# Kernel optimization log

Measured on AMD Instinct MI355X. Metric: run time of the kernel, lower is better.

The kernel has to match this reference:

```python
import jax, jax.numpy as jnp
import numpy as np

WIND_SIZE = 5
EPSILON = 1e-5
ALPHA = 1.0


def _windows(a, w):
    # a: [B,1,H,W] -> [B, w*w, H, W], zero-padded, window index in (di,dj) row-major
    # order matching torch's unfold(dim=2).unfold(dim=3) + reshape.
    p = w // 2
    B, _, H, W = a.shape
    ap = jnp.pad(a[:, 0], ((0, 0), (p, p), (p, p)))
    taps = [ap[:, i:i + H, j:j + W] for i in range(w) for j in range(w)]
    return jnp.stack(taps, axis=1)


def setup_inputs() -> dict:
    key = jax.random.key(0)
    ks = jax.random.split(key, 6)
    B, H, W = 4, 512, 512
    ww = WIND_SIZE * WIND_SIZE
    fake = jax.random.uniform(ks[0], (B, 1, H, W), dtype=jnp.float32)
    gamma_hdr = jax.random.uniform(ks[1], (B, 1, H, W), dtype=jnp.float32)
    # strictly positive so hdr**(1-f) is well defined
    hdr_original_im = jax.random.uniform(ks[2], (B, 1, H, W), dtype=jnp.float32) + 0.01
    r_weights = jax.random.uniform(ks[3], (B, ww, H, W), dtype=jnp.float32)
    # f_factors in [0.5, 1.5] to avoid division blow-up, realistic gamma factors
    f_factors = jax.random.uniform(ks[4], (B,), dtype=jnp.float32) + 0.5
    hdr_original_gray = jax.random.uniform(ks[5], (B, 1, H, W), dtype=jnp.float32)
    return {
        'fake': fake,
        'gamma_hdr': gamma_hdr,
        'hdr_original_im': hdr_original_im,
        'r_weights': r_weights,
        'f_factors': f_factors,
        'hdr_original_gray': hdr_original_gray,
    }


def reference(fake, gamma_hdr, hdr_original_im, r_weights, f_factors, hdr_original_gray):
    w = WIND_SIZE
    eps = jnp.float32(EPSILON)
    # create_window -> uniform window, normalized: every tap weight = 1/(w*w)
    dist_gauss = jnp.float32(1.0 / (w * w))
    weights_map = dist_gauss * r_weights                      # [B, w*w, H, W]
    weights_map_sum = jnp.sum(weights_map, axis=1, keepdims=True)  # [B,1,H,W]

    def bf_stats(x):
        xw = _windows(x, w)                                   # [B, w*w, H, W]
        mu = jnp.sum(xw * weights_map, axis=1, keepdims=True) / weights_map_sum
        var = jnp.sum((xw - mu) ** 2 * weights_map, axis=1, keepdims=True) / weights_map_sum
        std = jnp.sqrt(jnp.maximum(var, 0.0) + eps)
        return mu, std

    _, std_fake = bf_stats(fake)
    _, std_gamma = bf_stats(gamma_hdr)

    ff = f_factors[:, None, None, None]                       # [B,1,1,1]
    hdr_pow = jnp.power(hdr_original_im, 1.0 - ff)
    hw = _windows(hdr_pow, w)
    hdr_pow_mu = jnp.sum(hw * weights_map, axis=1, keepdims=True) / weights_map_sum

    w_blf = jnp.sum(r_weights, axis=1, keepdims=True) - 1.0   # [B,1,H,W]

    std_objective = (ALPHA / ff) * std_gamma * (hdr_pow_mu + eps)
    gray_max = jnp.max(hdr_original_gray.reshape(hdr_original_gray.shape[0], -1), axis=1)
    std_objective = std_objective * gray_max[:, None, None, None]

    res = 1.0 - std_fake / (std_fake + jax.lax.stop_gradient(std_objective))
    res = res * (w_blf / jnp.mean(w_blf))
    return jnp.mean(res)
```

## Files before the change

### kernel.cpp

```cpp
#include <hip/hip_runtime.h>

#define Bn 4
#define Hn 512
#define Wn 512
#define HWn (Hn * Wn)

constexpr float kEps = 1e-5f;


__global__ __launch_bounds__(256) void gmax_kernel(
    const float* __restrict__ gray, float* __restrict__ gpart) {
  const int b = blockIdx.y;
  const int i = (blockIdx.x * 256 + threadIdx.x) << 2;
  const float4 g4 = *(const float4*)(gray + b * HWn + i);
  float lmax = fmaxf(fmaxf(g4.x, g4.y), fmaxf(g4.z, g4.w));
#pragma unroll
  for (int off = 32; off > 0; off >>= 1)
    lmax = fmaxf(lmax, __shfl_down(lmax, off));
  __shared__ float smax[4];
  const int lane = threadIdx.x & 63, wid = threadIdx.x >> 6;
  if (lane == 0) smax[wid] = lmax;
  __syncthreads();
  if (threadIdx.x == 0) {
    gpart[b * 256 + blockIdx.x] =
        fmaxf(fmaxf(smax[0], smax[1]), fmaxf(smax[2], smax[3]));
  }
}

__global__ __launch_bounds__(512, 4) void main_kernel(
    const float* __restrict__ fake, const float* __restrict__ gamma,
    const float* __restrict__ hdr, const float* __restrict__ rw,
    const float* __restrict__ ff, const float* __restrict__ gpart,
    float* __restrict__ s1part, float* __restrict__ s2part) {
  __shared__ float smem[3][8][512];
  __shared__ float sh1[8], sh2[8], sh_gm[4];

  const int b = blockIdx.x >> 7;
  const int h0 = (blockIdx.x & 127) << 2;
  const float e = 1.0f - ff[b];

  const float* fb = fake + (size_t)b * HWn;
  const float* gb = gamma + (size_t)b * HWn;
  const float* hb = hdr + (size_t)b * HWn;

  const int t = threadIdx.x;
  const int lr = t >> 7;
  const int w0 = (t & 127) << 2;
  const int h = h0 + lr;
  const float* rwb = rw + (size_t)b * 25 * HWn + (h << 9) + w0;

  float4 wv[5];
#pragma unroll
  for (int d = 0; d < 5; ++d)
    wv[d] = *(const float4*)(rwb + (size_t)d * HWn);

  if (t < 256) {
    float gm = gpart[(b << 8) + t];
#pragma unroll
    for (int off = 32; off > 0; off >>= 1)
      gm = fmaxf(gm, __shfl_down(gm, off));
    if ((t & 63) == 0) sh_gm[t >> 6] = gm;
  }

  float4* smem4 = (float4*)smem;
#pragma unroll
  for (int k = 0; k < 6; ++k) {
    const int i = t + (k << 9);
    const int a = i >> 10;
    const int rem = i & 1023;
    const int r = rem >> 7;
    const int c4 = rem & 127;
    const int grow = min(max(h0 - 2 + r, 0), Hn - 1);
    const float* src = (a == 0) ? fb : (a == 1) ? gb : hb;
    float4 v = *(const float4*)(src + (grow << 9) + (c4 << 2));
    if (a == 2) {
      v.x = __powf(v.x, e);
      v.y = __powf(v.y, e);
      v.z = __powf(v.z, e);
      v.w = __powf(v.w, e);
    }
    smem4[i] = v;
  }
  __syncthreads();

  float Sw[4] = {0, 0, 0, 0}, Sf[4] = {0, 0, 0, 0}, Sf2[4] = {0, 0, 0, 0};
  float Sg[4] = {0, 0, 0, 0}, Sg2[4] = {0, 0, 0, 0}, Sh[4] = {0, 0, 0, 0};

  float cm[12];
#pragma unroll
  for (int i = 2; i < 10; ++i)
    cm[i] = ((unsigned)(w0 - 4 + i) < (unsigned)Wn) ? 1.0f : 0.0f;
  const int c0 = max(w0 - 4, 0);
  const int c2 = min(w0 + 4, Wn - 4);

#pragma unroll
  for (int dyi = 0; dyi < 5; ++dyi) {
    const int r = lr + dyi;
    const float rmask = ((unsigned)(h + dyi - 2) < (unsigned)Hn) ? 1.0f : 0.0f;

    float4 wc[5];
#pragma unroll
    for (int d = 0; d < 5; ++d) wc[d] = wv[d];
    if (dyi < 4) {
#pragma unroll
      for (int d = 0; d < 5; ++d)
        wv[d] = *(const float4*)(rwb + (size_t)((dyi + 1) * 5 + d) * HWn);
    }

    const float4 f0 = *(const float4*)&smem[0][r][c0];
    const float4 f1 = *(const float4*)&smem[0][r][w0];
    const float4 f2 = *(const float4*)&smem[0][r][c2];
    const float4 g0 = *(const float4*)&smem[1][r][c0];
    const float4 g1 = *(const float4*)&smem[1][r][w0];
    const float4 g2 = *(const float4*)&smem[1][r][c2];
    const float4 p0 = *(const float4*)&smem[2][r][c0];
    const float4 p1 = *(const float4*)&smem[2][r][w0];
    const float4 p2 = *(const float4*)&smem[2][r][c2];

    float xf[12] = {f0.x, f0.y, f0.z, f0.w, f1.x, f1.y, f1.z, f1.w,
                    f2.x, f2.y, f2.z, f2.w};
    float xg[12] = {g0.x, g0.y, g0.z, g0.w, g1.x, g1.y, g1.z, g1.w,
                    g2.x, g2.y, g2.z, g2.w};
    float xh[12] = {p0.x, p0.y, p0.z, p0.w, p1.x, p1.y, p1.z, p1.w,
                    p2.x, p2.y, p2.z, p2.w};
#pragma unroll
    for (int i2 = 2; i2 < 10; ++i2) {
      const float m = rmask * cm[i2];
      xf[i2] *= m;
      xg[i2] *= m;
      xh[i2] *= m;
    }
#pragma unroll
    for (int dxi = 0; dxi < 5; ++dxi) {
      const float wk[4] = {wc[dxi].x, wc[dxi].y, wc[dxi].z, wc[dxi].w};
#pragma unroll
      for (int j = 0; j < 4; ++j) {
        const float w = wk[j];
        const float f = xf[j + dxi + 2], g = xg[j + dxi + 2],
                    hp = xh[j + dxi + 2];
        Sw[j] += w;
        Sf[j] = fmaf(w, f, Sf[j]);
        Sf2[j] = fmaf(w * f, f, Sf2[j]);
        Sg[j] = fmaf(w, g, Sg[j]);
        Sg2[j] = fmaf(w * g, g, Sg2[j]);
        Sh[j] = fmaf(w, hp, Sh[j]);
      }
    }
  }

  const float ffb = ff[b];
  const float gmax =
      fmaxf(fmaxf(sh_gm[0], sh_gm[1]), fmaxf(sh_gm[2], sh_gm[3]));
  float s1 = 0.0f, s2 = 0.0f;
#pragma unroll
  for (int j = 0; j < 4; ++j) {
    const float invSw = 1.0f / Sw[j];
    const float muf = Sf[j] * invSw;
    const float varf = fmaxf(Sf2[j] * invSw - muf * muf, 0.0f);
    const float stdf = sqrtf(varf + kEps);
    const float mug = Sg[j] * invSw;
    const float varg = fmaxf(Sg2[j] * invSw - mug * mug, 0.0f);
    const float stdg = sqrtf(varg + kEps);
    const float hpmu = Sh[j] * invSw;
    const float stdobj = (1.0f / ffb) * stdg * (hpmu + kEps) * gmax;
    const float r = 1.0f - stdf / (stdf + stdobj);
    const float wblf = Sw[j] - 1.0f;
    s1 = fmaf(r, wblf, s1);
    s2 += wblf;
  }
#pragma unroll
  for (int off = 32; off > 0; off >>= 1) {
    s1 += __shfl_down(s1, off);
    s2 += __shfl_down(s2, off);
  }
  const int lane = t & 63, wid = t >> 6;
  if (lane == 0) {
    sh1[wid] = s1;
    sh2[wid] = s2;
  }
  __syncthreads();
  if (t == 0) {
    float a1 = 0.0f, a2 = 0.0f;
#pragma unroll
    for (int i = 0; i < 8; ++i) {
      a1 += sh1[i];
      a2 += sh2[i];
    }
    s1part[blockIdx.x] = a1;
    s2part[blockIdx.x] = a2;
  }
}

__global__ __launch_bounds__(512) void final_kernel(
    const float* __restrict__ s1part, const float* __restrict__ s2part,
    float* __restrict__ out) {
  const int t = threadIdx.x;
  float s1 = s1part[t];
  float s2 = s2part[t];
#pragma unroll
  for (int off = 32; off > 0; off >>= 1) {
    s1 += __shfl_down(s1, off);
    s2 += __shfl_down(s2, off);
  }
  __shared__ float sh1[8], sh2[8];
  const int lane = t & 63, wid = t >> 6;
  if (lane == 0) {
    sh1[wid] = s1;
    sh2[wid] = s2;
  }
  __syncthreads();
  if (t == 0) {
    float a1 = 0.0f, a2 = 0.0f;
#pragma unroll
    for (int i = 0; i < 8; ++i) {
      a1 += sh1[i];
      a2 += sh2[i];
    }
    out[0] = a1 / a2;
  }
}

extern "C" void kernel_launch(void* const* d_in, const int* in_sizes, int n_in,
                              void* d_out, int out_size, void* d_ws,
                              size_t ws_size, hipStream_t stream) {
  const float* fake = (const float*)d_in[0];
  const float* gamma = (const float*)d_in[1];
  const float* hdr = (const float*)d_in[2];
  const float* rw = (const float*)d_in[3];
  const float* ff = (const float*)d_in[4];
  const float* gray = (const float*)d_in[5];
  float* out = (float*)d_out;
  float* ws = (float*)d_ws;
  float* gpart = ws;
  float* s1part = ws + 1024;
  float* s2part = ws + 1536;

  gmax_kernel<<<dim3(256, Bn), 256, 0, stream>>>(gray, gpart);
  main_kernel<<<Bn * Hn / 4, 512, 0, stream>>>(fake, gamma, hdr, rw, ff, gpart,
                                               s1part, s2part);
  final_kernel<<<1, 512, 0, stream>>>(s1part, s2part, out);
}
```

Baseline: 176.7 us.

## Pad shared tiles with zero halo and stagger weight-plane reads per wave

The shared-memory tiles gain a zero-filled 4-column halo (row stride 520), so boundary handling becomes plain contiguous float4 reads with no per-element masking. Each wavefront starts the row loop at a different offset, so concurrent wavefronts read different r_weights planes at the same time, which is meant to spread DRAM channel and page traffic. The FMA form is also reshuffled to reuse w*f and w*g. In exchange the staging loop does more index division and some padded loads, and the row rotation makes the loop index depend on a runtime value.

```diff
diff --git a/kernel.cpp b/kernel.cpp
--- a/kernel.cpp
+++ b/kernel.cpp
@@ -32,7 +32,7 @@
     const float* __restrict__ hdr, const float* __restrict__ rw,
     const float* __restrict__ ff, const float* __restrict__ gpart,
     float* __restrict__ s1part, float* __restrict__ s2part) {
-  __shared__ float smem[3][8][512];
+  __shared__ float smem[3][8][520];
   __shared__ float sh1[8], sh2[8], sh_gm[4];
 
   const int b = blockIdx.x >> 7;
@@ -48,11 +48,12 @@
   const int w0 = (t & 127) << 2;
   const int h = h0 + lr;
   const float* rwb = rw + (size_t)b * 25 * HWn + (h << 9) + w0;
+  const int rot = (t >> 6) % 5;
 
   float4 wv[5];
 #pragma unroll
   for (int d = 0; d < 5; ++d)
-    wv[d] = *(const float4*)(rwb + (size_t)d * HWn);
+    wv[d] = *(const float4*)(rwb + (size_t)(rot * 5 + d) * HWn);
 
   if (t < 256) {
     float gm = gpart[(b << 8) + t];
@@ -62,74 +63,69 @@
     if ((t & 63) == 0) sh_gm[t >> 6] = gm;
   }
 
-  float4* smem4 = (float4*)smem;
-#pragma unroll
-  for (int k = 0; k < 6; ++k) {
+#pragma unroll
+  for (int k = 0; k < 7; ++k) {
     const int i = t + (k << 9);
-    const int a = i >> 10;
-    const int rem = i & 1023;
-    const int r = rem >> 7;
-    const int c4 = rem & 127;
-    const int grow = min(max(h0 - 2 + r, 0), Hn - 1);
-    const float* src = (a == 0) ? fb : (a == 1) ? gb : hb;
-    float4 v = *(const float4*)(src + (grow << 9) + (c4 << 2));
-    if (a == 2) {
-      v.x = __powf(v.x, e);
-      v.y = __powf(v.y, e);
-      v.z = __powf(v.z, e);
-      v.w = __powf(v.w, e);
-    }
-    smem4[i] = v;
+    if (i < 3120) {
+      const int a = i / 1040;
+      const int rem = i - a * 1040;
+      const int r = rem / 130;
+      const int j = rem - r * 130;
+      const int grow = h0 - 2 + r;
+      const bool ok =
+          ((unsigned)grow < (unsigned)Hn) && (j >= 1) && (j <= 128);
+      const int gr = min(max(grow, 0), Hn - 1);
+      const int gc = min(max(j - 1, 0), 127) << 2;
+      const float* src = (a == 0) ? fb : (a == 1) ? gb : hb;
+      float4 v = *(const float4*)(src + (gr << 9) + gc);
+      if (a == 2) {
+        v.x = __powf(v.x, e);
+        v.y = __powf(v.y, e);
+        v.z = __powf(v.z, e);
+        v.w = __powf(v.w, e);
+      }
+      if (!ok) v = make_float4(0.f, 0.f, 0.f, 0.f);
+      *(float4*)&smem[a][r][j << 2] = v;
+    }
   }
   __syncthreads();
 
   float Sw[4] = {0, 0, 0, 0}, Sf[4] = {0, 0, 0, 0}, Sf2[4] = {0, 0, 0, 0};
   float Sg[4] = {0, 0, 0, 0}, Sg2[4] = {0, 0, 0, 0}, Sh[4] = {0, 0, 0, 0};
 
-  float cm[12];
-#pragma unroll
-  for (int i = 2; i < 10; ++i)
-    cm[i] = ((unsigned)(w0 - 4 + i) < (unsigned)Wn) ? 1.0f : 0.0f;
-  const int c0 = max(w0 - 4, 0);
-  const int c2 = min(w0 + 4, Wn - 4);
-
-#pragma unroll
-  for (int dyi = 0; dyi < 5; ++dyi) {
+#pragma unroll
+  for (int s = 0; s < 5; ++s) {
+    int dyi = rot + s;
+    if (dyi >= 5) dyi -= 5;
     const int r = lr + dyi;
-    const float rmask = ((unsigned)(h + dyi - 2) < (unsigned)Hn) ? 1.0f : 0.0f;
 
     float4 wc[5];
 #pragma unroll
     for (int d = 0; d < 5; ++d) wc[d] = wv[d];
-    if (dyi < 4) {
+    if (s < 4) {
+      int dn = dyi + 1;
+      if (dn >= 5) dn -= 5;
 #pragma unroll
       for (int d = 0; d < 5; ++d)
-        wv[d] = *(const float4*)(rwb + (size_t)((dyi + 1) * 5 + d) * HWn);
-    }
-
-    const float4 f0 = *(const float4*)&smem[0][r][c0];
-    const float4 f1 = *(const float4*)&smem[0][r][w0];
-    const float4 f2 = *(const float4*)&smem[0][r][c2];
-    const float4 g0 = *(const float4*)&smem[1][r][c0];
-    const float4 g1 = *(const float4*)&smem[1][r][w0];
-    const float4 g2 = *(const float4*)&smem[1][r][c2];
-    const float4 p0 = *(const float4*)&smem[2][r][c0];
-    const float4 p1 = *(const float4*)&smem[2][r][w0];
-    const float4 p2 = *(const float4*)&smem[2][r][c2];
-
-    float xf[12] = {f0.x, f0.y, f0.z, f0.w, f1.x, f1.y, f1.z, f1.w,
-                    f2.x, f2.y, f2.z, f2.w};
-    float xg[12] = {g0.x, g0.y, g0.z, g0.w, g1.x, g1.y, g1.z, g1.w,
-                    g2.x, g2.y, g2.z, g2.w};
-    float xh[12] = {p0.x, p0.y, p0.z, p0.w, p1.x, p1.y, p1.z, p1.w,
-                    p2.x, p2.y, p2.z, p2.w};
-#pragma unroll
-    for (int i2 = 2; i2 < 10; ++i2) {
-      const float m = rmask * cm[i2];
-      xf[i2] *= m;
-      xg[i2] *= m;
-      xh[i2] *= m;
-    }
+        wv[d] = *(const float4*)(rwb + (size_t)(dn * 5 + d) * HWn);
+    }
+
+    const float4 f0 = *(const float4*)&smem[0][r][w0];
+    const float4 f1 = *(const float4*)&smem[0][r][w0 + 4];
+    const float4 f2 = *(const float4*)&smem[0][r][w0 + 8];
+    const float4 g0 = *(const float4*)&smem[1][r][w0];
+    const float4 g1 = *(const float4*)&smem[1][r][w0 + 4];
+    const float4 g2 = *(const float4*)&smem[1][r][w0 + 8];
+    const float4 p0 = *(const float4*)&smem[2][r][w0];
+    const float4 p1 = *(const float4*)&smem[2][r][w0 + 4];
+    const float4 p2 = *(const float4*)&smem[2][r][w0 + 8];
+
+    const float xf[12] = {f0.x, f0.y, f0.z, f0.w, f1.x, f1.y, f1.z, f1.w,
+                          f2.x, f2.y, f2.z, f2.w};
+    const float xg[12] = {g0.x, g0.y, g0.z, g0.w, g1.x, g1.y, g1.z, g1.w,
+                          g2.x, g2.y, g2.z, g2.w};
+    const float xh[12] = {p0.x, p0.y, p0.z, p0.w, p1.x, p1.y, p1.z, p1.w,
+                          p2.x, p2.y, p2.z, p2.w};
 #pragma unroll
     for (int dxi = 0; dxi < 5; ++dxi) {
       const float wk[4] = {wc[dxi].x, wc[dxi].y, wc[dxi].z, wc[dxi].w};
@@ -139,10 +135,12 @@
         const float f = xf[j + dxi + 2], g = xg[j + dxi + 2],
                     hp = xh[j + dxi + 2];
         Sw[j] += w;
-        Sf[j] = fmaf(w, f, Sf[j]);
-        Sf2[j] = fmaf(w * f, f, Sf2[j]);
-        Sg[j] = fmaf(w, g, Sg[j]);
-        Sg2[j] = fmaf(w * g, g, Sg2[j]);
+        const float wf = w * f;
+        Sf[j] += wf;
+        Sf2[j] = fmaf(wf, f, Sf2[j]);
+        const float wg = w * g;
+        Sg[j] += wg;
+        Sg2[j] = fmaf(wg, g, Sg2[j]);
         Sh[j] = fmaf(w, hp, Sh[j]);
       }
     }
```

Measured after the change: 179.0 us. No clear change (+1.3%).
